# Performance work log

Measured on AMD Instinct MI355X. Metric: run time of the kernel, lower is better.

## Reference

```python
import jax, jax.numpy as jnp
import numpy as np

VOCAB = 50257
FEAT = 512
EPS = 1e-12  # F.normalize default eps


def setup_inputs() -> dict:
    key = jax.random.key(0)
    k1, k2, k3 = jax.random.split(key, 3)
    token_ids = jax.random.randint(k1, (32, 4096), 0, VOCAB)
    # nn.Linear(vocab, feat): weight [FEAT, VOCAB], bias [FEAT]
    W = jax.random.normal(k2, (FEAT, VOCAB), dtype=jnp.float32) * 0.02
    b = jax.random.normal(k3, (FEAT,), dtype=jnp.float32) * 0.02
    return {"token_ids": token_ids, "W": W, "b": b}


def reference(token_ids, W, b):
    # one_hot(ids) @ W.T + b  ==  gather rows of W.T at ids, then add bias
    feats = W.T[token_ids] + b  # [B, S, FEAT]
    norm = jnp.sqrt(jnp.sum(feats * feats, axis=-1, keepdims=True))
    return feats / jnp.maximum(norm, EPS)
```

## Files before the change

### kernel.cpp

```cpp
#include <hip/hip_runtime.h>
#include <hip/hip_bf16.h>

#define VOCAB 50257
#define FEAT 512
#define NTOK (32 * 4096)
#define EPS 1e-12f

typedef float f32x4 __attribute__((ext_vector_type(4)));

__device__ __forceinline__ unsigned short f2bf(float x) {
    __hip_bfloat16 h = __float2bfloat16(x);
    unsigned short u;
    __builtin_memcpy(&u, &h, 2);
    return u;
}

__device__ __forceinline__ float bflo(unsigned int w) {
    unsigned int u = w << 16;
    float f;
    __builtin_memcpy(&f, &u, 4);
    return f;
}
__device__ __forceinline__ float bfhi(unsigned int w) {
    unsigned int u = w & 0xffff0000u;
    float f;
    __builtin_memcpy(&f, &u, 4);
    return f;
}

__global__ __launch_bounds__(256) void transpose_bias_bf16(
        const float* __restrict__ W, const float* __restrict__ b,
        unsigned short* __restrict__ Wt) {
    __shared__ float tile[64][65];
    const int t  = threadIdx.x;
    const int l  = t & 63;
    const int w  = t >> 6;
    const int v0 = blockIdx.x * 64;
    const int f0 = blockIdx.y * 64;

    const int  v_in = v0 + l;
    const bool vok  = v_in < VOCAB;
#pragma unroll
    for (int k = 0; k < 16; ++k) {
        const int fl = w * 16 + k;
        const int f  = f0 + fl;
        const float x = vok ? W[(size_t)f * VOCAB + v_in] : 0.0f;
        tile[fl][l] = x + b[f];
    }
    __syncthreads();

#pragma unroll
    for (int p = 0; p < 2; ++p) {
        const int idx = t + 256 * p;
        const int vl  = idx >> 3;
        const int ch  = idx & 7;
        const int v   = v0 + vl;
        if (v < VOCAB) {
            unsigned int pk[4];
#pragma unroll
            for (int j = 0; j < 4; ++j) {
                const int f = ch * 8 + 2 * j;
                pk[j] = (unsigned int)f2bf(tile[f][vl]) |
                        ((unsigned int)f2bf(tile[f + 1][vl]) << 16);
            }
            *(uint4*)(Wt + (size_t)v * FEAT + f0 + ch * 8) =
                make_uint4(pk[0], pk[1], pk[2], pk[3]);
        }
    }
}

__global__ __launch_bounds__(256) void encode_bf16(
        const int* __restrict__ ids, const unsigned short* __restrict__ Wt,
        float* __restrict__ out) {
    const int tok  = (int)((blockIdx.x * (unsigned long long)blockDim.x + threadIdx.x) >> 6);
    const int lane = threadIdx.x & 63;
    if (tok >= NTOK) return;

    const int id = ids[tok];
    const uint4 r = *(const uint4*)(Wt + (size_t)id * FEAT + lane * 8);

    float x[8];
    x[0] = bflo(r.x); x[1] = bfhi(r.x);
    x[2] = bflo(r.y); x[3] = bfhi(r.y);
    x[4] = bflo(r.z); x[5] = bfhi(r.z);
    x[6] = bflo(r.w); x[7] = bfhi(r.w);

    float s = 0.0f;
#pragma unroll
    for (int j = 0; j < 8; ++j) s += x[j] * x[j];
#pragma unroll
    for (int off = 32; off > 0; off >>= 1)
        s += __shfl_xor(s, off, 64);

    const float inv = 1.0f / fmaxf(sqrtf(s), EPS);

    f32x4 o0 = {x[0] * inv, x[1] * inv, x[2] * inv, x[3] * inv};
    f32x4 o1 = {x[4] * inv, x[5] * inv, x[6] * inv, x[7] * inv};
    f32x4* dst = (f32x4*)(out + (size_t)tok * FEAT + lane * 8);
    __builtin_nontemporal_store(o0, dst);
    __builtin_nontemporal_store(o1, dst + 1);
}

__global__ __launch_bounds__(256) void encode_direct(const int* __restrict__ ids,
                                                     const float* __restrict__ W,
                                                     const float* __restrict__ bias,
                                                     float* __restrict__ out) {
    const int tok  = (int)((blockIdx.x * (unsigned long long)blockDim.x + threadIdx.x) >> 6);
    const int lane = threadIdx.x & 63;
    if (tok >= NTOK) return;

    const int id = ids[tok];
    float x[8];
    float s = 0.0f;
#pragma unroll
    for (int j = 0; j < 8; ++j) {
        const int f = lane * 8 + j;
        x[j] = W[(size_t)f * VOCAB + id] + bias[f];
        s += x[j] * x[j];
    }
#pragma unroll
    for (int off = 32; off > 0; off >>= 1)
        s += __shfl_xor(s, off, 64);

    const float inv = 1.0f / fmaxf(sqrtf(s), EPS);
    float4 o0 = make_float4(x[0] * inv, x[1] * inv, x[2] * inv, x[3] * inv);
    float4 o1 = make_float4(x[4] * inv, x[5] * inv, x[6] * inv, x[7] * inv);
    float4* dst = (float4*)(out + (size_t)tok * FEAT + lane * 8);
    dst[0] = o0;
    dst[1] = o1;
}

extern "C" void kernel_launch(void* const* d_in, const int* in_sizes, int n_in,
                              void* d_out, int out_size, void* d_ws, size_t ws_size,
                              hipStream_t stream) {
    const int*   ids  = (const int*)d_in[0];
    const float* W    = (const float*)d_in[1];
    const float* bias = (const float*)d_in[2];
    float*       out  = (float*)d_out;

    const size_t wt_bytes = (size_t)VOCAB * FEAT * sizeof(unsigned short);
    const int nblocks = NTOK / 4;

    if (ws_size >= wt_bytes) {
        unsigned short* Wt = (unsigned short*)d_ws;
        dim3 tgrid((VOCAB + 63) / 64, FEAT / 64);
        transpose_bias_bf16<<<tgrid, 256, 0, stream>>>(W, bias, Wt);
        encode_bf16<<<nblocks, 256, 0, stream>>>(ids, Wt, out);
    } else {
        encode_direct<<<nblocks, 256, 0, stream>>>(ids, W, bias, out);
    }
}
```

Before: 133.6 us.

## Precompute per-vocab squared norms in transpose pass, vectorize W loads

The transpose kernel now also computes, for each vocab row, partial sums of squared bf16-rounded feature values. It writes them to a workspace array with one slice per 64-feature block. The encode kernel sums the 8 partials per token instead of doing a wave-wide shuffle reduction, which removes the cross-lane reduction from the per-token path. The transpose kernel also switches to 16-byte vectorized loads of W. This adds extra per-token scattered reads of the partial array, plus more work and workspace in the transpose kernel.

```diff
diff --git a/kernel.cpp b/kernel.cpp
--- a/kernel.cpp
+++ b/kernel.cpp
@@ -5,6 +5,7 @@
 #define FEAT 512
 #define NTOK (32 * 4096)
 #define EPS 1e-12f
+#define NFT 8
 
 typedef float f32x4 __attribute__((ext_vector_type(4)));
 
@@ -14,44 +15,72 @@
     __builtin_memcpy(&u, &h, 2);
     return u;
 }
-
+__device__ __forceinline__ float bfround(float x) {
+    return __bfloat162float(__float2bfloat16(x));
+}
 __device__ __forceinline__ float bflo(unsigned int w) {
-    unsigned int u = w << 16;
-    float f;
-    __builtin_memcpy(&f, &u, 4);
-    return f;
+    unsigned int u = w << 16; float f; __builtin_memcpy(&f, &u, 4); return f;
 }
 __device__ __forceinline__ float bfhi(unsigned int w) {
-    unsigned int u = w & 0xffff0000u;
-    float f;
-    __builtin_memcpy(&f, &u, 4);
-    return f;
+    unsigned int u = w & 0xffff0000u; float f; __builtin_memcpy(&f, &u, 4); return f;
 }
 
 __global__ __launch_bounds__(256) void transpose_bias_bf16(
         const float* __restrict__ W, const float* __restrict__ b,
-        unsigned short* __restrict__ Wt) {
+        unsigned short* __restrict__ Wt, float* __restrict__ partial) {
     __shared__ float tile[64][65];
+    __shared__ float psum[4][64];
     const int t  = threadIdx.x;
     const int l  = t & 63;
     const int w  = t >> 6;
     const int v0 = blockIdx.x * 64;
     const int f0 = blockIdx.y * 64;
+    const int c  = l & 15;
+    const int r  = l >> 4;
+    const int vb = v0 + c * 4;
 
-    const int  v_in = v0 + l;
-    const bool vok  = v_in < VOCAB;
+    float p[4] = {0.f, 0.f, 0.f, 0.f};
 #pragma unroll
-    for (int k = 0; k < 16; ++k) {
-        const int fl = w * 16 + k;
+    for (int k = 0; k < 4; ++k) {
+        const int fl = w * 16 + k * 4 + r;
         const int f  = f0 + fl;
-        const float x = vok ? W[(size_t)f * VOCAB + v_in] : 0.0f;
-        tile[fl][l] = x + b[f];
+        f32x4 x;
+        if (vb + 3 < VOCAB) {
+            __builtin_memcpy(&x, W + (size_t)f * VOCAB + vb, 16);
+        } else {
+#pragma unroll
+            for (int i = 0; i < 4; ++i)
+                x[i] = (vb + i < VOCAB) ? W[(size_t)f * VOCAB + vb + i] : 0.0f;
+        }
+        const float bf = b[f];
+#pragma unroll
+        for (int i = 0; i < 4; ++i) {
+            const float xi = x[i] + bf;
+            tile[fl][c * 4 + i] = xi;
+            const float xr = bfround(xi);
+            p[i] += xr * xr;
+        }
+    }
+
+#pragma unroll
+    for (int i = 0; i < 4; ++i) {
+        float s = p[i];
+        s += __shfl_xor(s, 16, 64);
+        s += __shfl_xor(s, 32, 64);
+        if (r == 0) psum[w][c * 4 + i] = s;
     }
     __syncthreads();
 
+    if (t < 64) {
+        const int v = v0 + t;
+        if (v < VOCAB)
+            partial[blockIdx.y * VOCAB + v] =
+                psum[0][t] + psum[1][t] + psum[2][t] + psum[3][t];
+    }
+
 #pragma unroll
-    for (int p = 0; p < 2; ++p) {
-        const int idx = t + 256 * p;
+    for (int ps = 0; ps < 2; ++ps) {
+        const int idx = t + 256 * ps;
         const int vl  = idx >> 3;
         const int ch  = idx & 7;
         const int v   = v0 + vl;
@@ -71,28 +100,25 @@
 
 __global__ __launch_bounds__(256) void encode_bf16(
         const int* __restrict__ ids, const unsigned short* __restrict__ Wt,
-        float* __restrict__ out) {
+        const float* __restrict__ partial, float* __restrict__ out) {
     const int tok  = (int)((blockIdx.x * (unsigned long long)blockDim.x + threadIdx.x) >> 6);
     const int lane = threadIdx.x & 63;
     if (tok >= NTOK) return;
 
     const int id = ids[tok];
-    const uint4 r = *(const uint4*)(Wt + (size_t)id * FEAT + lane * 8);
-
-    float x[8];
-    x[0] = bflo(r.x); x[1] = bfhi(r.x);
-    x[2] = bflo(r.y); x[3] = bfhi(r.y);
-    x[4] = bflo(r.z); x[5] = bfhi(r.z);
-    x[6] = bflo(r.w); x[7] = bfhi(r.w);
+    const uint4 rr = *(const uint4*)(Wt + (size_t)id * FEAT + lane * 8);
 
     float s = 0.0f;
 #pragma unroll
-    for (int j = 0; j < 8; ++j) s += x[j] * x[j];
-#pragma unroll
-    for (int off = 32; off > 0; off >>= 1)
-        s += __shfl_xor(s, off, 64);
+    for (int j = 0; j < NFT; ++j) s += partial[j * VOCAB + id];
 
     const float inv = 1.0f / fmaxf(sqrtf(s), EPS);
+
+    float x[8];
+    x[0] = bflo(rr.x); x[1] = bfhi(rr.x);
+    x[2] = bflo(rr.y); x[3] = bfhi(rr.y);
+    x[4] = bflo(rr.z); x[5] = bfhi(rr.z);
+    x[6] = bflo(rr.w); x[7] = bfhi(rr.w);
 
     f32x4 o0 = {x[0] * inv, x[1] * inv, x[2] * inv, x[3] * inv};
     f32x4 o1 = {x[4] * inv, x[5] * inv, x[6] * inv, x[7] * inv};
@@ -138,14 +164,16 @@
     const float* bias = (const float*)d_in[2];
     float*       out  = (float*)d_out;
 
-    const size_t wt_bytes = (size_t)VOCAB * FEAT * sizeof(unsigned short);
+    const size_t wt_bytes   = (size_t)VOCAB * FEAT * sizeof(unsigned short);
+    const size_t part_bytes = (size_t)NFT * VOCAB * sizeof(float);
     const int nblocks = NTOK / 4;
 
-    if (ws_size >= wt_bytes) {
+    if (ws_size >= wt_bytes + part_bytes) {
         unsigned short* Wt = (unsigned short*)d_ws;
+        float* partial     = (float*)((char*)d_ws + wt_bytes);
         dim3 tgrid((VOCAB + 63) / 64, FEAT / 64);
-        transpose_bias_bf16<<<tgrid, 256, 0, stream>>>(W, bias, Wt);
-        encode_bf16<<<nblocks, 256, 0, stream>>>(ids, Wt, out);
+        transpose_bias_bf16<<<tgrid, 256, 0, stream>>>(W, bias, Wt, partial);
+        encode_bf16<<<nblocks, 256, 0, stream>>>(ids, Wt, partial, out);
     } else {
         encode_direct<<<nblocks, 256, 0, stream>>>(ids, W, bias, out);
     }
```

New measurement: 123.4 us. -7.7%, faster.
